# Performance work log

Measured on AMD Instinct MI355X. Metric: run time of the kernel, lower is better.

The kernel has to match this reference:

```python
import jax, jax.numpy as jnp
import numpy as np
from jax import lax

FIRE_RATE = 0.5       # forward() default fire_rate
INPUT_CHANNELS = 1    # module input_channels
EPS = 1e-5            # BatchNorm eps


def p4_conv_z2(x, w, b):
    """Z2 -> P4 group conv. x: [B,I,H,W], w: [O,I,k,k] -> [B,O,4,H,W]."""
    # rotate the spatial kernel by r*90deg for each of the 4 output orientations
    ws = jnp.stack([jnp.rot90(w, r, axes=(2, 3)) for r in range(4)], axis=1)  # [O,4,I,k,k]
    O, _, I, k, _ = ws.shape
    y = lax.conv_general_dilated(x, ws.reshape(O * 4, I, k, k), (1, 1), 'SAME',
                                 dimension_numbers=('NCHW', 'OIHW', 'NCHW'))
    B, _, H, W = x.shape
    return y.reshape(B, O, 4, H, W) + b[None, :, None, None, None]


def p4_conv_p4(x, w, b):
    """P4 -> P4 group conv. x: [B,I,4,H,W], w: [O,I,4,k,k] -> [B,O,4,H,W]."""
    # for output orientation r: cyclic-shift input-orientation axis by r and rotate spatially by r
    ws = jnp.stack([jnp.rot90(jnp.roll(w, r, axis=2), r, axes=(3, 4)) for r in range(4)],
                   axis=1)  # [O,4,I,4,k,k]
    O, _, I, _, k, _ = ws.shape
    B, _, _, H, W = x.shape
    y = lax.conv_general_dilated(x.reshape(B, I * 4, H, W),
                                 ws.reshape(O * 4, I * 4, k, k), (1, 1), 'SAME',
                                 dimension_numbers=('NCHW', 'OIHW', 'NCHW'))
    return y.reshape(B, O, 4, H, W) + b[None, :, None, None, None]


def _update(x_nhwc, w1, b1, gamma, beta, w2, b2, key):
    x = jnp.transpose(x_nhwc, (0, 3, 1, 2))            # [B,C,H,W]
    y = p4_conv_z2(x, w1, b1)                          # [B,Ch,4,H,W]
    # BatchNorm3d (batch stats, affine): normalize each channel over (B, rot, H, W)
    mu = jnp.mean(y, axis=(0, 2, 3, 4), keepdims=True)
    var = jnp.var(y, axis=(0, 2, 3, 4), keepdims=True)
    y = gamma[None, :, None, None, None] * (y - mu) * lax.rsqrt(var + EPS) \
        + beta[None, :, None, None, None]
    y = jax.nn.relu(y)
    dy = p4_conv_p4(y, w2, b2).mean(axis=2)            # mean over rotation axis -> [B,C,H,W]
    B, _, H, W = dy.shape
    mask = (jax.random.uniform(key, (B, 1, H, W), dtype=dy.dtype) > FIRE_RATE).astype(dy.dtype)
    x = x + dy * mask
    return jnp.transpose(x, (0, 2, 3, 1))              # back to [B,H,W,C]


def nca_forward(x, w1, b1, gamma, beta, w2, b2, steps):
    base_key = jax.random.key(42)
    for step in range(steps):
        x2 = _update(x, w1, b1, gamma, beta, w2, b2, jax.random.fold_in(base_key, step))
        # first input_channels are clamped to the original input
        x = jnp.concatenate((x[..., :INPUT_CHANNELS], x2[..., INPUT_CHANNELS:]), axis=-1)
    return x


def setup_inputs() -> dict:
    key = jax.random.key(0)
    ks = jax.random.split(key, 6)
    B, H, W = 8, 192, 192
    C = 16            # channel_n
    CH = 128 // 8     # base_hidden_size = hidden_size // 8
    K = 7             # kernel_size
    # fan-in scaled init (matches nn.Conv2d-style scaling)
    x = jax.random.normal(ks[0], (B, H, W, C), dtype=jnp.float32)
    w1 = jax.random.normal(ks[1], (CH, C, K, K), dtype=jnp.float32) / np.sqrt(C * K * K)
    b1 = jnp.zeros((CH,), dtype=jnp.float32)
    gamma = jnp.ones((CH,), dtype=jnp.float32)
    beta = jnp.zeros((CH,), dtype=jnp.float32)
    w2 = jax.random.normal(ks[2], (C, CH, 4, 1, 1), dtype=jnp.float32) / np.sqrt(CH * 4)
    b2 = jnp.zeros((C,), dtype=jnp.float32)
    return {"x": x, "w1": w1, "b1": b1, "gamma": gamma, "beta": beta,
            "w2": w2, "b2": b2, "steps": 10}


def reference(x, w1, b1, gamma, beta, w2, b2, steps):
    return nca_forward(x, w1, b1, gamma, beta, w2, b2, steps)
```

## Files before the change

### kernel.cpp

```cpp
#include <hip/hip_runtime.h>
#include <stdint.h>

#define HH 192
#define WW 192
#define BB 8
#define NSTEP 10
#define HWSZ (HH*WW)
#define NPIX (BB*HWSZ)
#define TILE_W 24
#define TILE_H 16
#define XROWS 22
#define XCOLS 30
#define RSU   488
#define XBUFU (XROWS*RSU)
#define NKS   25
#define NBLK  (8*12*8)

typedef _Float16 f16x8 __attribute__((ext_vector_type(8)));
typedef float    f32x4 __attribute__((ext_vector_type(4)));

union PackU { ushort u[8]; uint4 v; };

__host__ __device__ inline void tf2x32(uint32_t k0, uint32_t k1,
                                       uint32_t x0, uint32_t x1,
                                       uint32_t &o0, uint32_t &o1) {
  const uint32_t k2 = k0 ^ k1 ^ 0x1BD11BDAu;
  x0 += k0; x1 += k1;
#define TFR(r) { x0 += x1; x1 = (x1 << (r)) | (x1 >> (32 - (r))); x1 ^= x0; }
  TFR(13) TFR(15) TFR(26) TFR(6)
  x0 += k1; x1 += k2 + 1u;
  TFR(17) TFR(29) TFR(16) TFR(24)
  x0 += k2; x1 += k0 + 2u;
  TFR(13) TFR(15) TFR(26) TFR(6)
  x0 += k0; x1 += k1 + 3u;
  TFR(17) TFR(29) TFR(16) TFR(24)
  x0 += k1; x1 += k2 + 4u;
  TFR(13) TFR(15) TFR(26) TFR(6)
  x0 += k2; x1 += k0 + 5u;
#undef TFR
  o0 = x0; o1 = x1;
}

__device__ inline void split2048(float v, ushort &h, ushort &l) {
  _Float16 hi = (_Float16)v;
  float r = (v - (float)hi) * 2048.0f;
  _Float16 lo = (_Float16)r;
  h = __builtin_bit_cast(ushort, hi);
  l = __builtin_bit_cast(ushort, lo);
}

__global__ void k_prep_wfrag(const float* __restrict__ w1,
                             ushort* __restrict__ wfh, ushort* __restrict__ wfl) {
  int idx = blockIdx.x * 256 + threadIdx.x;
  if (idx >= NKS * 4 * 64) return;
  const int lane = idx & 63;
  const int sm = idx >> 6;
  const int s = sm >> 2, mt = sm & 3;
  const int m = lane & 15, g = lane >> 4;
  const int j = mt * 16 + m, co = j >> 2, r = j & 3;
  const int t = 2 * s + (g >> 1);
  PackU ph, pl;
#pragma unroll
  for (int e = 0; e < 8; ++e) {
    const int ci = 8 * (g & 1) + e;
    float wv = 0.f;
    if (t < 49) {
      const int ky = t / 7, kx = t - (t / 7) * 7;
      int a = ky, b = kx;
      for (int i = 0; i < r; ++i) { int na = b, nb = 6 - a; a = na; b = nb; }
      wv = w1[((co * 16 + ci) * 7 + a) * 7 + b];
    }
    split2048(wv, ph.u[e], pl.u[e]);
  }
  ((uint4*)wfh)[sm * 64 + lane] = ph.v;
  ((uint4*)wfl)[sm * 64 + lane] = pl.v;
}

__global__ void k_prep_w2(const float* __restrict__ w2, float* __restrict__ wsum) {
  int idx = threadIdx.x;
  float s = 0.f;
  for (int t = 0; t < 4; ++t) s += w2[idx * 4 + t];
  wsum[idx] = 0.25f * s;
}

__global__ __launch_bounds__(512, 2) void k_conv1(
    const float* __restrict__ xsrc,
    const ushort* __restrict__ wfh,
    const ushort* __restrict__ wfl,
    const float* __restrict__ b1,
    float* __restrict__ y,
    float* __restrict__ partials)
{
  __shared__ __align__(16) ushort xsm[2 * XBUFU];
  __shared__ float red2[8][32];
  const int tid = threadIdx.x;
  const int lane = tid & 63, wid = tid >> 6;
  const int x0 = blockIdx.x * TILE_W, y0 = blockIdx.y * TILE_H;
  const int b = blockIdx.z;

  for (int p = tid; p < XROWS * XCOLS * 2; p += 512) {
    const int half = p & 1, t2 = p >> 1;
    const int lr = t2 / XCOLS, lc = t2 - (t2 / XCOLS) * XCOLS;
    const int gy = y0 + lr - 3, gx = x0 + lc - 3;
    float4 v0, v1;
    if ((unsigned)gy < (unsigned)HH && (unsigned)gx < (unsigned)WW) {
      const float4* px = (const float4*)(xsrc + ((size_t)b * HWSZ + (size_t)gy * WW + gx) * 16 + half * 8);
      v0 = px[0]; v1 = px[1];
    } else {
      v0 = v1 = make_float4(0.f, 0.f, 0.f, 0.f);
    }
    const float xv[8] = {v0.x, v0.y, v0.z, v0.w, v1.x, v1.y, v1.z, v1.w};
    PackU h, l;
#pragma unroll
    for (int c = 0; c < 8; ++c) split2048(xv[c], h.u[c], l.u[c]);
    const int ub = lr * RSU + lc * 16 + half * 8;
    *(uint4*)&xsm[ub] = h.v;
    *(uint4*)&xsm[XBUFU + ub] = l.v;
  }
  __syncthreads();

  const int n = lane & 15;
  const int q = lane >> 4;
  const int h = q & 1;
  const int bU0 = n * RSU + (3 * wid + 0) * 16 + h * 8;
  const int bU1 = bU0 + 16;
  const int bU2 = bU0 + 32;

  const f16x8* __restrict__ WAh = (const f16x8*)wfh;
  const f16x8* __restrict__ WAl = (const f16x8*)wfl;

  float bias[4];
#pragma unroll
  for (int mt = 0; mt < 4; ++mt) bias[mt] = b1[mt * 4 + q];

  f32x4 accH[3][4], accC[3][4];
#pragma unroll
  for (int st = 0; st < 3; ++st)
#pragma unroll
    for (int mt = 0; mt < 4; ++mt) {
      const float bv = bias[mt];
      accH[st][mt] = (f32x4){bv, bv, bv, bv};
      accC[st][mt] = (f32x4){0.f, 0.f, 0.f, 0.f};
    }

  f16x8 Ah[2][4], Al[2][4];
  f16x8 Bh[2][3], Bl[2][3];

#pragma unroll
  for (int mt = 0; mt < 4; ++mt) {
    Ah[0][mt] = WAh[mt * 64 + lane];
    Al[0][mt] = WAl[mt * 64 + lane];
  }
  {
    const int off = (lane < 32) ? 0 : 16;
    Bh[0][0] = *(const f16x8*)&xsm[bU0 + off];
    Bl[0][0] = *(const f16x8*)&xsm[XBUFU + bU0 + off];
    Bh[0][1] = *(const f16x8*)&xsm[bU1 + off];
    Bl[0][1] = *(const f16x8*)&xsm[XBUFU + bU1 + off];
    Bh[0][2] = *(const f16x8*)&xsm[bU2 + off];
    Bl[0][2] = *(const f16x8*)&xsm[XBUFU + bU2 + off];
  }

#pragma unroll
  for (int s = 0; s < NKS; ++s) {
    const int cb = s & 1, nb = cb ^ 1;
    if (s < NKS - 1) {
#pragma unroll
      for (int mt = 0; mt < 4; ++mt) {
        const int f = ((s + 1) * 4 + mt) * 64 + lane;
        Ah[nb][mt] = WAh[f];
        Al[nb][mt] = WAl[f];
      }
      const int t0 = 2 * (s + 1), t1 = t0 + 1;
      const int o0 = (t0 / 7) * RSU + (t0 % 7) * 16;
      const int o1 = (t1 < 49) ? (t1 / 7) * RSU + (t1 % 7) * 16 : 0;
      const int off = (lane < 32) ? o0 : o1;
      Bh[nb][0] = *(const f16x8*)&xsm[bU0 + off];
      Bl[nb][0] = *(const f16x8*)&xsm[XBUFU + bU0 + off];
      Bh[nb][1] = *(const f16x8*)&xsm[bU1 + off];
      Bl[nb][1] = *(const f16x8*)&xsm[XBUFU + bU1 + off];
      Bh[nb][2] = *(const f16x8*)&xsm[bU2 + off];
      Bl[nb][2] = *(const f16x8*)&xsm[XBUFU + bU2 + off];
    }
    __builtin_amdgcn_sched_barrier(0);
#pragma unroll
    for (int mt = 0; mt < 4; ++mt) {
#pragma unroll
      for (int st = 0; st < 3; ++st)
        accH[st][mt] = __builtin_amdgcn_mfma_f32_16x16x32_f16(Ah[cb][mt], Bh[cb][st], accH[st][mt], 0, 0, 0);
    }
#pragma unroll
    for (int mt = 0; mt < 4; ++mt) {
#pragma unroll
      for (int st = 0; st < 3; ++st)
        accC[st][mt] = __builtin_amdgcn_mfma_f32_16x16x32_f16(Ah[cb][mt], Bl[cb][st], accC[st][mt], 0, 0, 0);
    }
#pragma unroll
    for (int mt = 0; mt < 4; ++mt) {
#pragma unroll
      for (int st = 0; st < 3; ++st)
        accC[st][mt] = __builtin_amdgcn_mfma_f32_16x16x32_f16(Al[cb][mt], Bh[cb][st], accC[st][mt], 0, 0, 0);
    }
  }

  float sC[4] = {0.f, 0.f, 0.f, 0.f}, qC[4] = {0.f, 0.f, 0.f, 0.f};
#pragma unroll
  for (int st = 0; st < 3; ++st) {
    const size_t pix = (size_t)b * HWSZ + (size_t)(y0 + n) * WW + (x0 + 3 * wid + st);
#pragma unroll
    for (int mt = 0; mt < 4; ++mt) {
      f32x4 res = accH[st][mt] + accC[st][mt] * 4.8828125e-4f;
      *(float4*)(y + pix * 64 + mt * 16 + q * 4) =
          make_float4(res[0], res[1], res[2], res[3]);
#pragma unroll
      for (int r = 0; r < 4; ++r) { sC[mt] += res[r]; qC[mt] += res[r] * res[r]; }
    }
  }
#pragma unroll
  for (int mt = 0; mt < 4; ++mt) {
    float s = sC[mt], s2 = qC[mt];
#pragma unroll
    for (int off = 1; off <= 8; off <<= 1) {
      s += __shfl_xor(s, off); s2 += __shfl_xor(s2, off);
    }
    if (n == 0) {
      red2[wid][(mt * 4 + q) * 2] = s;
      red2[wid][(mt * 4 + q) * 2 + 1] = s2;
    }
  }
  __syncthreads();
  if (tid < 32) {
    float v = 0.f;
#pragma unroll
    for (int w2i = 0; w2i < 8; ++w2i) v += red2[w2i][tid];
    const int blk = (b * gridDim.y + blockIdx.y) * gridDim.x + blockIdx.x;
    partials[(size_t)blk * 32 + tid] = v;
  }
}

__global__ __launch_bounds__(256) void k_bnstats(
    const float* __restrict__ partials,
    const float* __restrict__ gamma, const float* __restrict__ beta,
    float* __restrict__ stats)
{
  const int c = blockIdx.x;
  const int tid = threadIdx.x;
  float s = 0.f, s2 = 0.f;
  for (int i = tid; i < NBLK; i += 256) {
    s  += partials[(size_t)i * 32 + 2 * c];
    s2 += partials[(size_t)i * 32 + 2 * c + 1];
  }
  __shared__ float rs[256], rs2[256];
  rs[tid] = s; rs2[tid] = s2;
  __syncthreads();
  for (int off = 128; off > 0; off >>= 1) {
    if (tid < off) { rs[tid] += rs[tid + off]; rs2[tid] += rs2[tid + off]; }
    __syncthreads();
  }
  if (tid == 0) {
    const float N = (float)BB * 4.f * HH * WW;
    const float mu = rs[0] / N;
    const float var = rs2[0] / N - mu * mu;
    const float rstd = rsqrtf(var + 1e-5f);
    const float sc = gamma[c] * rstd;
    stats[2 * c]     = sc;
    stats[2 * c + 1] = beta[c] - mu * sc;
  }
}

__global__ __launch_bounds__(256) void k_update(
    const float* __restrict__ xsrc,
    const float* __restrict__ y,
    const float* __restrict__ stats,
    const float* __restrict__ wsum,
    const float* __restrict__ b2,
    float* __restrict__ xdst,
    uint32_t fk0, uint32_t fk1)
{
  __shared__ float sss[32];
  __shared__ float sws[256];
  __shared__ float sb2[16];
  const int tid = threadIdx.x;
  sws[tid] = wsum[tid];
  if (tid < 32) sss[tid] = stats[tid];
  if (tid < 16) sb2[tid] = b2[tid];
  __syncthreads();

  const size_t pix = (size_t)blockIdx.x * 256 + tid;
  const float4* yp = (const float4*)(y + pix * 64);
  float ysum[16];
#pragma unroll
  for (int c = 0; c < 16; ++c) {
    const float4 v = yp[c];
    const float sc = sss[2 * c], sh = sss[2 * c + 1];
    ysum[c] = fmaxf(fmaf(sc, v.x, sh), 0.f) + fmaxf(fmaf(sc, v.y, sh), 0.f)
            + fmaxf(fmaf(sc, v.z, sh), 0.f) + fmaxf(fmaf(sc, v.w, sh), 0.f);
  }

  uint32_t h0, h1;
  tf2x32(fk0, fk1, 0u, (uint32_t)pix, h0, h1);
  const uint32_t bits = h0 ^ h1;
  const float u = __uint_as_float((bits >> 9) | 0x3f800000u) - 1.0f;
  const float m = (u > 0.5f) ? 1.0f : 0.0f;

  const float4* xp = (const float4*)(xsrc + pix * 16);
  float4* op = (float4*)(xdst + pix * 16);
#pragma unroll
  for (int qq = 0; qq < 4; ++qq) {
    const float4 xv = xp[qq];
    float d[4];
#pragma unroll
    for (int jj = 0; jj < 4; ++jj) {
      const int o = 4 * qq + jj;
      float s = sb2[o];
#pragma unroll
      for (int c = 0; c < 16; ++c) s = fmaf(sws[o * 16 + c], ysum[c], s);
      d[jj] = s;
    }
    float4 r;
    r.x = xv.x + d[0] * m;
    r.y = xv.y + d[1] * m;
    r.z = xv.z + d[2] * m;
    r.w = xv.w + d[3] * m;
    if (qq == 0) r.x = xv.x;
    op[qq] = r;
  }
}

extern "C" void kernel_launch(void* const* d_in, const int* in_sizes, int n_in,
                              void* d_out, int out_size, void* d_ws, size_t ws_size,
                              hipStream_t stream) {
  const float* x_in  = (const float*)d_in[0];
  const float* w1    = (const float*)d_in[1];
  const float* b1    = (const float*)d_in[2];
  const float* gamma = (const float*)d_in[3];
  const float* beta  = (const float*)d_in[4];
  const float* w2    = (const float*)d_in[5];
  const float* b2    = (const float*)d_in[6];
  float* out = (float*)d_out;

  float* ws       = (float*)d_ws;
  float* y        = ws;
  ushort* wfh     = (ushort*)(y + (size_t)NPIX * 64);
  ushort* wfl     = wfh + NKS * 2048;
  float* wsum     = (float*)(wfl + NKS * 2048);
  float* partials = wsum + 256;
  float* stats    = partials + NBLK * 32;

  k_prep_wfrag<<<NKS, 256, 0, stream>>>(w1, wfh, wfl);
  k_prep_w2<<<1, 256, 0, stream>>>(w2, wsum);

  for (int s = 0; s < NSTEP; ++s) {
    const float* xsrc = (s == 0) ? x_in : out;
    k_conv1<<<dim3(WW / TILE_W, HH / TILE_H, BB), 512, 0, stream>>>(xsrc, wfh, wfl, b1, y, partials);
    k_bnstats<<<16, 256, 0, stream>>>(partials, gamma, beta, stats);
    uint32_t fk0, fk1;
    tf2x32(0u, 42u, 0u, (uint32_t)s, fk0, fk1);
    k_update<<<NPIX / 256, 256, 0, stream>>>(xsrc, y, stats, wsum, b2, out, fk0, fk1);
  }
}
```

Before: 1.095 ms.

## Halve conv1 block to 4 waves, each computing 6 output columns

The conv1 kernel now runs 256 threads per block (4 waves) instead of 512, and each wave covers 6 output column strips instead of 3. The per-wave weight fragments (A operands) are reused across twice as many MFMA tiles, which halves redundant global weight loads per block and increases MFMA work per load. The cost is that accumulator and B-operand register use doubles (48 f32x4 accumulators plus 24 B fragments), which may spill or reduce occupancy. The launch bound is now (256,1), and fewer waves are resident to hide LDS latency.

```diff
diff --git a/kernel.cpp b/kernel.cpp
--- a/kernel.cpp
+++ b/kernel.cpp
@@ -83,7 +83,7 @@
   wsum[idx] = 0.25f * s;
 }
 
-__global__ __launch_bounds__(512, 2) void k_conv1(
+__global__ __launch_bounds__(256, 1) void k_conv1(
     const float* __restrict__ xsrc,
     const ushort* __restrict__ wfh,
     const ushort* __restrict__ wfl,
@@ -92,13 +92,14 @@
     float* __restrict__ partials)
 {
   __shared__ __align__(16) ushort xsm[2 * XBUFU];
-  __shared__ float red2[8][32];
+  __shared__ float red2[4][32];
   const int tid = threadIdx.x;
   const int lane = tid & 63, wid = tid >> 6;
   const int x0 = blockIdx.x * TILE_W, y0 = blockIdx.y * TILE_H;
   const int b = blockIdx.z;
-
-  for (int p = tid; p < XROWS * XCOLS * 2; p += 512) {
+  const int bid = (b * gridDim.y + blockIdx.y) * gridDim.x + blockIdx.x;
+
+  for (int p = tid; p < XROWS * XCOLS * 2; p += 256) {
     const int half = p & 1, t2 = p >> 1;
     const int lr = t2 / XCOLS, lc = t2 - (t2 / XCOLS) * XCOLS;
     const int gy = y0 + lr - 3, gx = x0 + lc - 3;
@@ -122,9 +123,9 @@
   const int n = lane & 15;
   const int q = lane >> 4;
   const int h = q & 1;
-  const int bU0 = n * RSU + (3 * wid + 0) * 16 + h * 8;
-  const int bU1 = bU0 + 16;
-  const int bU2 = bU0 + 32;
+  int bU[6];
+#pragma unroll
+  for (int st = 0; st < 6; ++st) bU[st] = n * RSU + (6 * wid + st) * 16 + h * 8;
 
   const f16x8* __restrict__ WAh = (const f16x8*)wfh;
   const f16x8* __restrict__ WAl = (const f16x8*)wfl;
@@ -133,9 +134,9 @@
 #pragma unroll
   for (int mt = 0; mt < 4; ++mt) bias[mt] = b1[mt * 4 + q];
 
-  f32x4 accH[3][4], accC[3][4];
-#pragma unroll
-  for (int st = 0; st < 3; ++st)
+  f32x4 accH[6][4], accC[6][4];
+#pragma unroll
+  for (int st = 0; st < 6; ++st)
 #pragma unroll
     for (int mt = 0; mt < 4; ++mt) {
       const float bv = bias[mt];
@@ -144,7 +145,14 @@
     }
 
   f16x8 Ah[2][4], Al[2][4];
-  f16x8 Bh[2][3], Bl[2][3];
+  f16x8 Bh[2][6], Bl[2][6];
+
+  auto boff = [&](int sp) -> int {
+    const int t0 = 2 * sp, t1 = t0 + 1;
+    const int o0 = (t0 / 7) * RSU + (t0 % 7) * 16;
+    const int o1 = (t1 < 49) ? (t1 / 7) * RSU + (t1 % 7) * 16 : 0;
+    return (lane < 32) ? o0 : o1;
+  };
 
 #pragma unroll
   for (int mt = 0; mt < 4; ++mt) {
@@ -152,13 +160,12 @@
     Al[0][mt] = WAl[mt * 64 + lane];
   }
   {
-    const int off = (lane < 32) ? 0 : 16;
-    Bh[0][0] = *(const f16x8*)&xsm[bU0 + off];
-    Bl[0][0] = *(const f16x8*)&xsm[XBUFU + bU0 + off];
-    Bh[0][1] = *(const f16x8*)&xsm[bU1 + off];
-    Bl[0][1] = *(const f16x8*)&xsm[XBUFU + bU1 + off];
-    Bh[0][2] = *(const f16x8*)&xsm[bU2 + off];
-    Bl[0][2] = *(const f16x8*)&xsm[XBUFU + bU2 + off];
+    const int off = boff(0);
+#pragma unroll
+    for (int st = 0; st < 6; ++st) {
+      Bh[0][st] = *(const f16x8*)&xsm[bU[st] + off];
+      Bl[0][st] = *(const f16x8*)&xsm[XBUFU + bU[st] + off];
+    }
   }
 
 #pragma unroll
@@ -171,42 +178,38 @@
         Ah[nb][mt] = WAh[f];
         Al[nb][mt] = WAl[f];
       }
-      const int t0 = 2 * (s + 1), t1 = t0 + 1;
-      const int o0 = (t0 / 7) * RSU + (t0 % 7) * 16;
-      const int o1 = (t1 < 49) ? (t1 / 7) * RSU + (t1 % 7) * 16 : 0;
-      const int off = (lane < 32) ? o0 : o1;
-      Bh[nb][0] = *(const f16x8*)&xsm[bU0 + off];
-      Bl[nb][0] = *(const f16x8*)&xsm[XBUFU + bU0 + off];
-      Bh[nb][1] = *(const f16x8*)&xsm[bU1 + off];
-      Bl[nb][1] = *(const f16x8*)&xsm[XBUFU + bU1 + off];
-      Bh[nb][2] = *(const f16x8*)&xsm[bU2 + off];
-      Bl[nb][2] = *(const f16x8*)&xsm[XBUFU + bU2 + off];
+      const int off = boff(s + 1);
+#pragma unroll
+      for (int st = 0; st < 6; ++st) {
+        Bh[nb][st] = *(const f16x8*)&xsm[bU[st] + off];
+        Bl[nb][st] = *(const f16x8*)&xsm[XBUFU + bU[st] + off];
+      }
     }
     __builtin_amdgcn_sched_barrier(0);
 #pragma unroll
     for (int mt = 0; mt < 4; ++mt) {
 #pragma unroll
-      for (int st = 0; st < 3; ++st)
+      for (int st = 0; st < 6; ++st)
         accH[st][mt] = __builtin_amdgcn_mfma_f32_16x16x32_f16(Ah[cb][mt], Bh[cb][st], accH[st][mt], 0, 0, 0);
     }
 #pragma unroll
     for (int mt = 0; mt < 4; ++mt) {
 #pragma unroll
-      for (int st = 0; st < 3; ++st)
+      for (int st = 0; st < 6; ++st)
         accC[st][mt] = __builtin_amdgcn_mfma_f32_16x16x32_f16(Ah[cb][mt], Bl[cb][st], accC[st][mt], 0, 0, 0);
     }
 #pragma unroll
     for (int mt = 0; mt < 4; ++mt) {
 #pragma unroll
-      for (int st = 0; st < 3; ++st)
+      for (int st = 0; st < 6; ++st)
         accC[st][mt] = __builtin_amdgcn_mfma_f32_16x16x32_f16(Al[cb][mt], Bh[cb][st], accC[st][mt], 0, 0, 0);
     }
   }
 
   float sC[4] = {0.f, 0.f, 0.f, 0.f}, qC[4] = {0.f, 0.f, 0.f, 0.f};
 #pragma unroll
-  for (int st = 0; st < 3; ++st) {
-    const size_t pix = (size_t)b * HWSZ + (size_t)(y0 + n) * WW + (x0 + 3 * wid + st);
+  for (int st = 0; st < 6; ++st) {
+    const size_t pix = (size_t)b * HWSZ + (size_t)(y0 + n) * WW + (x0 + 6 * wid + st);
 #pragma unroll
     for (int mt = 0; mt < 4; ++mt) {
       f32x4 res = accH[st][mt] + accC[st][mt] * 4.8828125e-4f;
@@ -230,11 +233,8 @@
   }
   __syncthreads();
   if (tid < 32) {
-    float v = 0.f;
-#pragma unroll
-    for (int w2i = 0; w2i < 8; ++w2i) v += red2[w2i][tid];
-    const int blk = (b * gridDim.y + blockIdx.y) * gridDim.x + blockIdx.x;
-    partials[(size_t)blk * 32 + tid] = v;
+    float v = red2[0][tid] + red2[1][tid] + red2[2][tid] + red2[3][tid];
+    partials[(size_t)bid * 32 + tid] = v;
   }
 }
 
@@ -352,7 +352,7 @@
 
   for (int s = 0; s < NSTEP; ++s) {
     const float* xsrc = (s == 0) ? x_in : out;
-    k_conv1<<<dim3(WW / TILE_W, HH / TILE_H, BB), 512, 0, stream>>>(xsrc, wfh, wfl, b1, y, partials);
+    k_conv1<<<dim3(WW / TILE_W, HH / TILE_H, BB), 256, 0, stream>>>(xsrc, wfh, wfl, b1, y, partials);
     k_bnstats<<<16, 256, 0, stream>>>(partials, gamma, beta, stats);
     uint32_t fk0, fk1;
     tf2x32(0u, 42u, 0u, (uint32_t)s, fk0, fk1);
```

Result: no change. 1.077 ms (-1.7%).
